# Kernel tuning notes

Hardware: AMD Instinct MI355X
Metric: run time of the kernel (lower is better)

Reference implementation:

```python
import jax, jax.numpy as jnp
import numpy as np

NUM_NODES = 94
SEQ_LEN = 784
OUT_CLASSES = 10
ALPHA = 0.5
GAMMA = 0.1
OMEGA = 2.0 * np.pi / 28.0
H = 1.0
INV_SQRT_N = 1.0 / np.sqrt(NUM_NODES)


def _xavier(key, shape):
    fan_in, fan_out = shape[1], shape[0]
    limit = np.sqrt(6.0 / (fan_in + fan_out))
    return jax.random.uniform(key, shape, jnp.float32, -limit, limit)


def setup_inputs() -> dict:
    key = jax.random.key(0)
    k_in, k_ih, k_hh, k_ro = jax.random.split(key, 4)
    batch = 1024
    return {
        "input_sequence": jax.random.normal(k_in, (batch, SEQ_LEN), jnp.float32),
        "w_ih": _xavier(k_ih, (NUM_NODES, 1)),   # Linear(1 -> N) weight
        "b_ih": jnp.zeros((NUM_NODES,), jnp.float32),
        "w_hh": _xavier(k_hh, (NUM_NODES, NUM_NODES)),  # Linear(N -> N) weight
        "b_hh": jnp.zeros((NUM_NODES,), jnp.float32),
        "w_ro": _xavier(k_ro, (OUT_CLASSES, NUM_NODES)),  # readout weight
        "b_ro": jnp.zeros((OUT_CLASSES,), jnp.float32),
    }


def reference(input_sequence, w_ih, b_ih, w_hh, b_hh, w_ro, b_ro):
    batch = input_sequence.shape[0]
    # precompute external drive for all steps: [T, B, N]
    # W_ih(s_t) with input_dim=1 is an outer product: s_t * w_ih[:,0] + b_ih
    s = input_sequence.T  # [T, B]
    w_ih_vec = w_ih[:, 0]  # [N]

    def step(carry, s_t):
        x, y = carry
        I_ext = s_t[:, None] * w_ih_vec[None, :] + b_ih  # [B, N]
        I_rec = y @ w_hh.T + b_hh                        # [B, N]
        A = (I_ext + I_rec) * INV_SQRT_N
        accel = ALPHA * jnp.tanh(A) - 2.0 * GAMMA * y - (OMEGA ** 2) * x
        x_new = x + H * y
        y_new = y + H * accel
        return (x_new, y_new), None

    x0 = jnp.zeros((batch, NUM_NODES), jnp.float32)
    y0 = jnp.zeros((batch, NUM_NODES), jnp.float32)
    (x_final, _), _ = jax.lax.scan(step, (x0, y0), s)
    return x_final @ w_ro.T + b_ro  # [B, 10]
```

## Files before the change

### kernel.cpp

```cpp
#include <hip/hip_runtime.h>
#include <math.h>

#define NUM_NODES 94
#define SEQ_LEN 784
#define OUT_CLASSES 10

#define TWO_GAMMA 0.2f
#define OM2 0.0503551324598949f
#define INV_SQRT_N 0.103142124625879
#define LOG2E 1.4426950408889634
#define WSCALE ((float)(2.0 * INV_SQRT_N * LOG2E))

typedef _Float16 h2 __attribute__((ext_vector_type(2)));
typedef _Float16 h4 __attribute__((ext_vector_type(4)));

__device__ __forceinline__ float dpp_xor1(float x) {
    return __int_as_float(__builtin_amdgcn_mov_dpp(__float_as_int(x), 0xB1, 0xF, 0xF, true));
}
__device__ __forceinline__ float dpp_xor2(float x) {
    return __int_as_float(__builtin_amdgcn_mov_dpp(__float_as_int(x), 0x4E, 0xF, 0xF, true));
}
__device__ __forceinline__ float dpp_mir8(float x) {
    return __int_as_float(__builtin_amdgcn_mov_dpp(__float_as_int(x), 0x141, 0xF, 0xF, true));
}

__device__ __forceinline__ float dot2(h2 a, h2 b, float c) {
#if __has_builtin(__builtin_amdgcn_fdot2)
    return __builtin_amdgcn_fdot2(a, b, c, false);
#else
    return c + (float)a[0] * (float)b[0] + (float)a[1] * (float)b[1];
#endif
}

__global__
__attribute__((amdgpu_flat_work_group_size(64, 64), amdgpu_waves_per_eu(1, 1)))
void horn_kernel(
    const float* __restrict__ input,
    const float* __restrict__ w_ih,
    const float* __restrict__ b_ih,
    const float* __restrict__ w_hh,
    const float* __restrict__ b_hh,
    const float* __restrict__ w_ro,
    const float* __restrict__ b_ro,
    float* __restrict__ out)
{
    __shared__ __align__(16) _Float16 ysh[96];
    __shared__ __align__(16) float    xsh[96];

    const int lane = threadIdx.x;
    const int g    = lane >> 3;
    const int lw   = lane & 7;
    const int bb   = blockIdx.x;

    const int b0  = lane & 1, b1 = (lane >> 1) & 1, b2v = (lane >> 2) & 1;
    const int c0i = b0 ^ b2v;
    const int c1i = b1 ^ b2v;
    const int c2i = b2v;

    const int row0 = 12 * g, col0 = 12 * lw;

    h2 w2[12][6];
    #pragma unroll
    for (int j = 0; j < 12; j++) {
        int rr;
        if (j < 8) {
            rr = row0 + 4 * (((j >> 2) & 1) ^ c2i)
                      + 2 * (((j >> 1) & 1) ^ c1i)
                      +     ((j & 1) ^ c0i);
        } else {
            const int jj = j - 8;
            rr = row0 + 8 + 2 * (((jj >> 1) & 1) ^ c1i)
                          +     ((jj & 1) ^ c0i);
        }
        #pragma unroll
        for (int c = 0; c < 12; c++) {
            const int cc = col0 + c;
            float v = (rr < NUM_NODES && cc < NUM_NODES)
                        ? w_hh[rr * NUM_NODES + cc] * WSCALE : 0.0f;
            w2[j][c >> 1][c & 1] = (_Float16)v;
        }
    }

    const int nA = row0 + 4 * c2i + 2 * c1i + c0i;
    const int nB = row0 + 8 + 2 * c1i + c0i;
    const float wihA  = (nA < NUM_NODES) ? w_ih[nA] * WSCALE : 0.0f;
    const float biasA = (nA < NUM_NODES) ? (b_ih[nA] + b_hh[nA]) * WSCALE : 0.0f;
    const float wihB  = (nB < NUM_NODES) ? w_ih[nB] * WSCALE : 0.0f;
    const float biasB = (nB < NUM_NODES) ? (b_ih[nB] + b_hh[nB]) * WSCALE : 0.0f;

    float xA = 0.0f, yA = 0.0f, xB = 0.0f, yB = 0.0f;

    ysh[nA] = (_Float16)0.0f;
    ysh[nB] = (_Float16)0.0f;
    asm volatile("s_waitcnt lgkmcnt(0)" ::: "memory");

    const float* srow = input + (size_t)bb * SEQ_LEN;
    float sc = srow[0];

    const h4* yv4 = (const h4*)&ysh[col0];

    for (int t = 0; t < SEQ_LEN; t++) {
        const int tn = (t + 1 < SEQ_LEN) ? t + 1 : (SEQ_LEN - 1);
        float sn = srow[tn];

        h4 Y0 = yv4[0], Y1 = yv4[1], Y2 = yv4[2];
        h2 yy0 = __builtin_shufflevector(Y0, Y0, 0, 1);
        h2 yy1 = __builtin_shufflevector(Y0, Y0, 2, 3);
        h2 yy2 = __builtin_shufflevector(Y1, Y1, 0, 1);
        h2 yy3 = __builtin_shufflevector(Y1, Y1, 2, 3);
        h2 yy4 = __builtin_shufflevector(Y2, Y2, 0, 1);
        h2 yy5 = __builtin_shufflevector(Y2, Y2, 2, 3);

        float P[12];
        #pragma unroll
        for (int i = 0; i < 12; i++) {
            float p = dot2(w2[i][0], yy0, 0.0f);
            p = dot2(w2[i][1], yy1, p);
            p = dot2(w2[i][2], yy2, p);
            p = dot2(w2[i][3], yy3, p);
            p = dot2(w2[i][4], yy4, p);
            p = dot2(w2[i][5], yy5, p);
            P[i] = p;
        }

        float Q0 = P[0]  + dpp_xor1(P[1]);
        float Q1 = P[2]  + dpp_xor1(P[3]);
        float Q2 = P[4]  + dpp_xor1(P[5]);
        float Q3 = P[6]  + dpp_xor1(P[7]);
        float Q4 = P[8]  + dpp_xor1(P[9]);
        float Q5 = P[10] + dpp_xor1(P[11]);
        float R0 = Q0 + dpp_xor2(Q1);
        float R1 = Q2 + dpp_xor2(Q3);
        float R2 = Q4 + dpp_xor2(Q5);
        float SA = R0 + dpp_mir8(R1);
        float SB = R2 + dpp_mir8(R2);

        float eA = __builtin_amdgcn_exp2f(fmaf(sc, wihA, biasA) + SA);
        float aA = 0.5f - __builtin_amdgcn_rcpf(eA + 1.0f);
        aA = fmaf(-TWO_GAMMA, yA, aA);
        aA = fmaf(-OM2, xA, aA);
        xA += yA;  yA += aA;

        float eB = __builtin_amdgcn_exp2f(fmaf(sc, wihB, biasB) + SB);
        float aB = 0.5f - __builtin_amdgcn_rcpf(eB + 1.0f);
        aB = fmaf(-TWO_GAMMA, yB, aB);
        aB = fmaf(-OM2, xB, aB);
        xB += yB;  yB += aB;

        ysh[nA] = (_Float16)yA;
        ysh[nB] = (_Float16)yB;
        asm volatile("s_waitcnt lgkmcnt(0)" ::: "memory");

        sc = sn;
    }

    xsh[nA] = xA;
    xsh[nB] = xB;
    asm volatile("s_waitcnt lgkmcnt(0)" ::: "memory");

    if (lane < OUT_CLASSES) {
        float acc = b_ro[lane];
        #pragma unroll 2
        for (int j = 0; j < NUM_NODES; j++) {
            acc += xsh[j] * w_ro[lane * NUM_NODES + j];
        }
        out[(size_t)bb * OUT_CLASSES + lane] = acc;
    }
}

extern "C" void kernel_launch(void* const* d_in, const int* in_sizes, int n_in,
                              void* d_out, int out_size, void* d_ws, size_t ws_size,
                              hipStream_t stream) {
    const float* input = (const float*)d_in[0];
    const float* w_ih  = (const float*)d_in[1];
    const float* b_ih  = (const float*)d_in[2];
    const float* w_hh  = (const float*)d_in[3];
    const float* b_hh  = (const float*)d_in[4];
    const float* w_ro  = (const float*)d_in[5];
    const float* b_ro  = (const float*)d_in[6];
    float* out = (float*)d_out;

    const int batch = in_sizes[0] / SEQ_LEN;
    dim3 grid(batch);
    dim3 block(64);

    hipLaunchKernelGGL(horn_kernel, grid, block, 0, stream,
                       input, w_ih, b_ih, w_hh, b_hh, w_ro, b_ro, out);
}
```

Baseline: 314.7 us.

## Process two batch elements per wavefront to interleave independent recurrences

```diff
diff --git a/kernel.cpp b/kernel.cpp
--- a/kernel.cpp
+++ b/kernel.cpp
@@ -44,13 +44,13 @@
     const float* __restrict__ b_ro,
     float* __restrict__ out)
 {
-    __shared__ __align__(16) _Float16 ysh[96];
-    __shared__ __align__(16) float    xsh[96];
+    __shared__ __align__(16) _Float16 ysh[2][96];
+    __shared__ __align__(16) float    xsh[2][96];
 
     const int lane = threadIdx.x;
     const int g    = lane >> 3;
     const int lw   = lane & 7;
-    const int bb   = blockIdx.x;
+    const int e0   = blockIdx.x * 2;
 
     const int b0  = lane & 1, b1 = (lane >> 1) & 1, b2v = (lane >> 2) & 1;
     const int c0i = b0 ^ b2v;
@@ -88,83 +88,119 @@
     const float wihB  = (nB < NUM_NODES) ? w_ih[nB] * WSCALE : 0.0f;
     const float biasB = (nB < NUM_NODES) ? (b_ih[nB] + b_hh[nB]) * WSCALE : 0.0f;
 
-    float xA = 0.0f, yA = 0.0f, xB = 0.0f, yB = 0.0f;
-
-    ysh[nA] = (_Float16)0.0f;
-    ysh[nB] = (_Float16)0.0f;
+    float xA0 = 0.f, yA0 = 0.f, xB0 = 0.f, yB0 = 0.f;
+    float xA1 = 0.f, yA1 = 0.f, xB1 = 0.f, yB1 = 0.f;
+
+    ysh[0][nA] = (_Float16)0.f;  ysh[0][nB] = (_Float16)0.f;
+    ysh[1][nA] = (_Float16)0.f;  ysh[1][nB] = (_Float16)0.f;
     asm volatile("s_waitcnt lgkmcnt(0)" ::: "memory");
 
-    const float* srow = input + (size_t)bb * SEQ_LEN;
-    float sc = srow[0];
-
-    const h4* yv4 = (const h4*)&ysh[col0];
+    const float* srow0 = input + (size_t)e0 * SEQ_LEN;
+    const float* srow1 = srow0 + SEQ_LEN;
+    float sc0 = srow0[0];
+    float sc1 = srow1[0];
+
+    const h4* yv0 = (const h4*)&ysh[0][col0];
+    const h4* yv1 = (const h4*)&ysh[1][col0];
 
     for (int t = 0; t < SEQ_LEN; t++) {
         const int tn = (t + 1 < SEQ_LEN) ? t + 1 : (SEQ_LEN - 1);
-        float sn = srow[tn];
-
-        h4 Y0 = yv4[0], Y1 = yv4[1], Y2 = yv4[2];
-        h2 yy0 = __builtin_shufflevector(Y0, Y0, 0, 1);
-        h2 yy1 = __builtin_shufflevector(Y0, Y0, 2, 3);
-        h2 yy2 = __builtin_shufflevector(Y1, Y1, 0, 1);
-        h2 yy3 = __builtin_shufflevector(Y1, Y1, 2, 3);
-        h2 yy4 = __builtin_shufflevector(Y2, Y2, 0, 1);
-        h2 yy5 = __builtin_shufflevector(Y2, Y2, 2, 3);
-
-        float P[12];
+        float sn0 = srow0[tn];
+        float sn1 = srow1[tn];
+
+        h4 Y00 = yv0[0], Y01 = yv0[1], Y02 = yv0[2];
+        h4 Y10 = yv1[0], Y11 = yv1[1], Y12 = yv1[2];
+        h2 a0 = __builtin_shufflevector(Y00, Y00, 0, 1);
+        h2 a1 = __builtin_shufflevector(Y00, Y00, 2, 3);
+        h2 a2 = __builtin_shufflevector(Y01, Y01, 0, 1);
+        h2 a3 = __builtin_shufflevector(Y01, Y01, 2, 3);
+        h2 a4 = __builtin_shufflevector(Y02, Y02, 0, 1);
+        h2 a5 = __builtin_shufflevector(Y02, Y02, 2, 3);
+        h2 b0v = __builtin_shufflevector(Y10, Y10, 0, 1);
+        h2 b1v = __builtin_shufflevector(Y10, Y10, 2, 3);
+        h2 b2w = __builtin_shufflevector(Y11, Y11, 0, 1);
+        h2 b3v = __builtin_shufflevector(Y11, Y11, 2, 3);
+        h2 b4v = __builtin_shufflevector(Y12, Y12, 0, 1);
+        h2 b5v = __builtin_shufflevector(Y12, Y12, 2, 3);
+
+        float P0[12], P1[12];
         #pragma unroll
         for (int i = 0; i < 12; i++) {
-            float p = dot2(w2[i][0], yy0, 0.0f);
-            p = dot2(w2[i][1], yy1, p);
-            p = dot2(w2[i][2], yy2, p);
-            p = dot2(w2[i][3], yy3, p);
-            p = dot2(w2[i][4], yy4, p);
-            p = dot2(w2[i][5], yy5, p);
-            P[i] = p;
-        }
-
-        float Q0 = P[0]  + dpp_xor1(P[1]);
-        float Q1 = P[2]  + dpp_xor1(P[3]);
-        float Q2 = P[4]  + dpp_xor1(P[5]);
-        float Q3 = P[6]  + dpp_xor1(P[7]);
-        float Q4 = P[8]  + dpp_xor1(P[9]);
-        float Q5 = P[10] + dpp_xor1(P[11]);
-        float R0 = Q0 + dpp_xor2(Q1);
-        float R1 = Q2 + dpp_xor2(Q3);
-        float R2 = Q4 + dpp_xor2(Q5);
-        float SA = R0 + dpp_mir8(R1);
-        float SB = R2 + dpp_mir8(R2);
-
-        float eA = __builtin_amdgcn_exp2f(fmaf(sc, wihA, biasA) + SA);
-        float aA = 0.5f - __builtin_amdgcn_rcpf(eA + 1.0f);
-        aA = fmaf(-TWO_GAMMA, yA, aA);
-        aA = fmaf(-OM2, xA, aA);
-        xA += yA;  yA += aA;
-
-        float eB = __builtin_amdgcn_exp2f(fmaf(sc, wihB, biasB) + SB);
-        float aB = 0.5f - __builtin_amdgcn_rcpf(eB + 1.0f);
-        aB = fmaf(-TWO_GAMMA, yB, aB);
-        aB = fmaf(-OM2, xB, aB);
-        xB += yB;  yB += aB;
-
-        ysh[nA] = (_Float16)yA;
-        ysh[nB] = (_Float16)yB;
+            float p = dot2(w2[i][0], a0, 0.0f);
+            float q = dot2(w2[i][0], b0v, 0.0f);
+            p = dot2(w2[i][1], a1, p);   q = dot2(w2[i][1], b1v, q);
+            p = dot2(w2[i][2], a2, p);   q = dot2(w2[i][2], b2w, q);
+            p = dot2(w2[i][3], a3, p);   q = dot2(w2[i][3], b3v, q);
+            p = dot2(w2[i][4], a4, p);   q = dot2(w2[i][4], b4v, q);
+            p = dot2(w2[i][5], a5, p);   q = dot2(w2[i][5], b5v, q);
+            P0[i] = p;  P1[i] = q;
+        }
+
+        float Q00 = P0[0]  + dpp_xor1(P0[1]);
+        float Q10 = P1[0]  + dpp_xor1(P1[1]);
+        float Q01 = P0[2]  + dpp_xor1(P0[3]);
+        float Q11 = P1[2]  + dpp_xor1(P1[3]);
+        float Q02 = P0[4]  + dpp_xor1(P0[5]);
+        float Q12 = P1[4]  + dpp_xor1(P1[5]);
+        float Q03 = P0[6]  + dpp_xor1(P0[7]);
+        float Q13 = P1[6]  + dpp_xor1(P1[7]);
+        float Q04 = P0[8]  + dpp_xor1(P0[9]);
+        float Q14 = P1[8]  + dpp_xor1(P1[9]);
+        float Q05 = P0[10] + dpp_xor1(P0[11]);
+        float Q15 = P1[10] + dpp_xor1(P1[11]);
+        float R00 = Q00 + dpp_xor2(Q01);
+        float R10 = Q10 + dpp_xor2(Q11);
+        float R01 = Q02 + dpp_xor2(Q03);
+        float R11 = Q12 + dpp_xor2(Q13);
+        float R02 = Q04 + dpp_xor2(Q05);
+        float R12 = Q14 + dpp_xor2(Q15);
+        float SA0 = R00 + dpp_mir8(R01);
+        float SA1 = R10 + dpp_mir8(R11);
+        float SB0 = R02 + dpp_mir8(R02);
+        float SB1 = R12 + dpp_mir8(R12);
+
+        float eA0 = __builtin_amdgcn_exp2f(fmaf(sc0, wihA, biasA) + SA0);
+        float eA1 = __builtin_amdgcn_exp2f(fmaf(sc1, wihA, biasA) + SA1);
+        float eB0 = __builtin_amdgcn_exp2f(fmaf(sc0, wihB, biasB) + SB0);
+        float eB1 = __builtin_amdgcn_exp2f(fmaf(sc1, wihB, biasB) + SB1);
+        float aA0 = 0.5f - __builtin_amdgcn_rcpf(eA0 + 1.0f);
+        float aA1 = 0.5f - __builtin_amdgcn_rcpf(eA1 + 1.0f);
+        float aB0 = 0.5f - __builtin_amdgcn_rcpf(eB0 + 1.0f);
+        float aB1 = 0.5f - __builtin_amdgcn_rcpf(eB1 + 1.0f);
+        aA0 = fmaf(-TWO_GAMMA, yA0, aA0);  aA0 = fmaf(-OM2, xA0, aA0);
+        aA1 = fmaf(-TWO_GAMMA, yA1, aA1);  aA1 = fmaf(-OM2, xA1, aA1);
+        aB0 = fmaf(-TWO_GAMMA, yB0, aB0);  aB0 = fmaf(-OM2, xB0, aB0);
+        aB1 = fmaf(-TWO_GAMMA, yB1, aB1);  aB1 = fmaf(-OM2, xB1, aB1);
+        xA0 += yA0;  yA0 += aA0;
+        xA1 += yA1;  yA1 += aA1;
+        xB0 += yB0;  yB0 += aB0;
+        xB1 += yB1;  yB1 += aB1;
+
+        ysh[0][nA] = (_Float16)yA0;
+        ysh[1][nA] = (_Float16)yA1;
+        ysh[0][nB] = (_Float16)yB0;
+        ysh[1][nB] = (_Float16)yB1;
         asm volatile("s_waitcnt lgkmcnt(0)" ::: "memory");
 
-        sc = sn;
+        sc0 = sn0;
+        sc1 = sn1;
     }
 
-    xsh[nA] = xA;
-    xsh[nB] = xB;
+    xsh[0][nA] = xA0;  xsh[0][nB] = xB0;
+    xsh[1][nA] = xA1;  xsh[1][nB] = xB1;
     asm volatile("s_waitcnt lgkmcnt(0)" ::: "memory");
 
-    if (lane < OUT_CLASSES) {
-        float acc = b_ro[lane];
-        #pragma unroll 2
-        for (int j = 0; j < NUM_NODES; j++) {
-            acc += xsh[j] * w_ro[lane * NUM_NODES + j];
-        }
-        out[(size_t)bb * OUT_CLASSES + lane] = acc;
+    {
+        const int e = lane >> 4;
+        const int c = lane & 15;
+        if (e < 2 && c < OUT_CLASSES) {
+            float acc = b_ro[c];
+            #pragma unroll 2
+            for (int j = 0; j < NUM_NODES; j++) {
+                acc += xsh[e][j] * w_ro[c * NUM_NODES + j];
+            }
+            out[(size_t)(e0 + e) * OUT_CLASSES + c] = acc;
+        }
     }
 }
 
@@ -181,7 +217,7 @@
     float* out = (float*)d_out;
 
     const int batch = in_sizes[0] / SEQ_LEN;
-    dim3 grid(batch);
+    dim3 grid(batch / 2);
     dim3 block(64);
 
     hipLaunchKernelGGL(horn_kernel, grid, block, 0, stream,
```

Measured after the change: 491.4 us. +56.1%, slower.
